# Kernel tuning notes

Measured on AMD Instinct MI355X. Metric: run time of the kernel, lower is better.

## Reference

```python
import jax, jax.numpy as jnp
import numpy as np

DIM = 256      # C
TOPK = 32      # topk_win_num
WIN = 8        # winSize
G = 64         # g (shift group size); 4*G == DIM here


def setup_inputs() -> dict:
    key = jax.random.key(0)
    k0, k1, k2, k3 = jax.random.split(key, 4)
    B, Nt, Ns, C = 32, 256, 4096, DIM
    z = jax.random.normal(k0, (B, Nt, C), jnp.float32)
    x = jax.random.normal(k1, (B, Ns, C), jnp.float32)
    # shift_op_down: Conv2d(C, 4g, 1) -> weight [4g, C]; shift_op_up: Conv2d(4g, C, 1)
    Wd = jax.random.normal(k2, (4 * G, C), jnp.float32) * 0.05
    bd = jnp.zeros((4 * G,), jnp.float32)
    Wu = jax.random.normal(k3, (C, 4 * G), jnp.float32) * 0.05
    bu = jnp.zeros((C,), jnp.float32)
    return {"z": z, "x": x, "Wd": Wd, "bd": bd, "Wu": Wu, "bu": bu}


def reference(z, x, Wd, bd, Wu, bu):
    B, Nt, C = z.shape
    Ns = x.shape[1]
    hs = int(np.sqrt(Ns))
    wn = hs // WIN          # windows per side
    wsa = WIN * WIN         # tokens per window
    K = TOPK

    # AdaptiveMaxPool2d((1,1)) over template tokens -> global max per channel
    z_max = jnp.max(z, axis=1)                               # [B, C]
    sim = jnp.einsum('bc,bnc->bn', z_max, x) / C             # [B, Ns]
    # per-window mean similarity
    sim = sim.reshape(B, wn, WIN, wn, WIN).transpose(0, 1, 3, 2, 4)
    sim = sim.reshape(B, wn * wn, wsa).mean(-1)              # [B, wn*wn]
    idx = jax.lax.top_k(sim, K)[1]                           # [B, K]

    # windowed view of search tokens: [B, wn*wn, wsa, C]
    x_win = x.reshape(B, wn, WIN, wn, WIN, C).transpose(0, 1, 3, 2, 4, 5)
    x_win = x_win.reshape(B, wn * wn, wsa, C)
    x_sel = jnp.take_along_axis(x_win, idx[:, :, None, None], axis=1)  # [B, K, wsa, C]

    xe = x_sel.reshape(B * K, WIN, WIN, C)                   # NHWC per selected window
    t = xe @ Wd.T + bd                                       # 1x1 conv down -> [n, h, w, 4G]

    # 4-direction spatial shift by 1 (zero fill), one channel group per direction
    g0, g1, g2, g3 = t[..., :G], t[..., G:2 * G], t[..., 2 * G:3 * G], t[..., 3 * G:]
    s0 = jnp.pad(g0[:, :, 1:, :], ((0, 0), (0, 0), (0, 1), (0, 0)))  # shift left  (W)
    s1 = jnp.pad(g1[:, :, :-1, :], ((0, 0), (0, 0), (1, 0), (0, 0)))  # shift right (W)
    s2 = jnp.pad(g2[:, 1:, :, :], ((0, 0), (0, 1), (0, 0), (0, 0)))  # shift up    (H)
    s3 = jnp.pad(g3[:, :-1, :, :], ((0, 0), (1, 0), (0, 0), (0, 0)))  # shift down  (H)
    sh = jnp.concatenate([s0, s1, s2, s3], axis=-1)          # [n, h, w, 4G]

    up = sh @ Wu.T + bu                                      # 1x1 conv up -> [n, h, w, C]
    out = (xe + up).reshape(B, K * WIN * WIN, C)             # [B, K*wsa, C]
    return out
```

## Files before the change

kernel.cpp:

```cpp
#include <hip/hip_runtime.h>
#include <hip/hip_bf16.h>

#define C_DIM 256
#define B_SZ 32
#define NS 4096
#define NT_Z 256
#define TOPK_K 32
#define NWIN 64
#define WTOK 64

typedef __attribute__((ext_vector_type(8))) short short8;
typedef __attribute__((ext_vector_type(4))) float f32x4;

static __device__ inline unsigned short f2b(float f) {
  union { float f; unsigned int u; } x; x.f = f;
  unsigned int u = x.u;
  return (unsigned short)((u + 0x7FFFu + ((u >> 16) & 1u)) >> 16);
}
static __device__ inline float b2f(unsigned int h16) {
  union { unsigned int u; float f; } x; x.u = h16 << 16;
  return x.f;
}

__global__ void prep_kernel(const float* __restrict__ Wd, const float* __restrict__ Wu,
                            unsigned short* __restrict__ Wdb, unsigned short* __restrict__ Wub,
                            const float* __restrict__ z, float* __restrict__ zpart) {
  int blk = blockIdx.x;
  if (blk < 64) {
    int i = blk * 256 + threadIdx.x;
    float4 a = ((const float4*)Wd)[i];
    float4 c = ((const float4*)Wu)[i];
    ushort4 ha, hc;
    ha.x = f2b(a.x); ha.y = f2b(a.y); ha.z = f2b(a.z); ha.w = f2b(a.w);
    hc.x = f2b(c.x); hc.y = f2b(c.y); hc.z = f2b(c.z); hc.w = f2b(c.w);
    ((ushort4*)Wdb)[i] = ha;
    ((ushort4*)Wub)[i] = hc;
  } else {
    int i = blk - 64;
    int b = i >> 3, ch = i & 7;
    int c = threadIdx.x;
    const float* p = z + ((size_t)b * NT_Z + ch * 32) * C_DIM + c;
    float m = p[0];
    for (int n = 1; n < 32; ++n) m = fmaxf(m, p[(size_t)n * C_DIM]);
    zpart[(size_t)i * C_DIM + c] = m;
  }
}

__global__ __launch_bounds__(256) void winscore_kernel(const float* __restrict__ x,
                                                       const float* __restrict__ zpart,
                                                       float* __restrict__ score) {
  int b = blockIdx.x >> 6;
  int w = blockIdx.x & 63;
  int wy = w >> 3, wx = w & 7;

  __shared__ float zs[C_DIM];
  {
    float m = zpart[(size_t)(b * 8) * C_DIM + threadIdx.x];
    #pragma unroll
    for (int ch = 1; ch < 8; ++ch)
      m = fmaxf(m, zpart[(size_t)(b * 8 + ch) * C_DIM + threadIdx.x]);
    zs[threadIdx.x] = m;
  }
  __syncthreads();

  int wv = threadIdx.x >> 6;
  int ln = threadIdx.x & 63;

  float a0 = 0.f, a1 = 0.f, a2 = 0.f, a3 = 0.f;
  for (int t = 0; t < 16; ++t) {
    int tok = wv * 16 + t;
    int iy = tok >> 3, ix = tok & 7;
    int n = (wy * 8 + iy) * 64 + wx * 8 + ix;
    const float4 v = *(const float4*)(x + ((size_t)b * NS + n) * C_DIM + ln * 4);
    a0 += v.x; a1 += v.y; a2 += v.z; a3 += v.w;
  }
  const float4 z4 = ((const float4*)zs)[ln];
  float p = a0 * z4.x + a1 * z4.y + a2 * z4.z + a3 * z4.w;
  for (int off = 32; off >= 1; off >>= 1) p += __shfl_xor(p, off);

  __shared__ float wsum[4];
  if (ln == 0) wsum[wv] = p;
  __syncthreads();
  if (threadIdx.x == 0) score[blockIdx.x] = wsum[0] + wsum[1] + wsum[2] + wsum[3];
}

__global__ __launch_bounds__(256, 2) void fused_win(
    const float* __restrict__ x, const float* __restrict__ score,
    const unsigned short* __restrict__ Wdb, const unsigned short* __restrict__ Wub,
    const float* __restrict__ bd, const float* __restrict__ bu,
    float* __restrict__ out)
{
  __shared__ unsigned short xe_s[WTOK * C_DIM];
  __shared__ unsigned short t_s[WTOK * C_DIM];
  __shared__ float sc[NWIN];
  __shared__ int wsel_s;

  const int bk = blockIdx.x;
  const int b = bk >> 5;
  const int kk = bk & 31;
  const int tid = threadIdx.x;

  if (tid < NWIN) sc[tid] = score[b * NWIN + tid];
  __syncthreads();
  if (tid < NWIN) {
    float v = sc[tid];
    int rank = 0;
    #pragma unroll
    for (int j = 0; j < NWIN; ++j) {
      float sj = sc[j];
      rank += (sj > v) || (sj == v && j < tid);
    }
    if (rank == kk) wsel_s = tid;
  }
  __syncthreads();
  const int wsel = wsel_s;
  const int wy = wsel >> 3, wx = wsel & 7;

  const int wv = tid >> 6;
  const int ln = tid & 63;
  const int lr = ln & 15;
  const int lg = ln >> 4;

  const unsigned short* wdbase = Wdb + ((wv * 4) * 16 + lr) * C_DIM + lg * 8;
  const unsigned short* wubase = Wub + ((wv * 4) * 16 + lr) * C_DIM + lg * 8;

  short8 wreg[8][4];
  #pragma unroll
  for (int ks = 0; ks < 8; ++ks)
    #pragma unroll
    for (int nt = 0; nt < 4; ++nt)
      wreg[ks][nt] = *(const short8*)(wdbase + nt * 16 * C_DIM + ks * 32);

  {
    const int c4 = tid & 63;
    const int m0 = tid >> 6;
    const float* xb = x + (size_t)b * NS * C_DIM + c4 * 4;
    float4 xv[16];
    #pragma unroll
    for (int i = 0; i < 16; ++i) {
      int m = m0 + i * 4;
      int n = (wy * 8 + (m >> 3)) * 64 + wx * 8 + (m & 7);
      xv[i] = *(const float4*)(xb + (size_t)n * C_DIM);
    }
    #pragma unroll
    for (int i = 0; i < 16; ++i) {
      int m = m0 + i * 4;
      ushort4 h;
      h.x = f2b(xv[i].x); h.y = f2b(xv[i].y); h.z = f2b(xv[i].z); h.w = f2b(xv[i].w);
      int byteoff = m * 512 + ((c4 * 8) ^ ((m & 7) << 4));
      *(ushort4*)((char*)xe_s + byteoff) = h;
    }
  }
  __syncthreads();

  f32x4 acc[4][4];
  #pragma unroll
  for (int a = 0; a < 4; ++a)
    #pragma unroll
    for (int n2 = 0; n2 < 4; ++n2) acc[a][n2] = (f32x4){0.f, 0.f, 0.f, 0.f};

  #pragma unroll
  for (int ks = 0; ks < 8; ++ks) {
    const int kb = ks * 64 + lg * 16;
    short8 af[4];
    #pragma unroll
    for (int mt = 0; mt < 4; ++mt) {
      int m = mt * 16 + lr;
      af[mt] = *(const short8*)((const char*)xe_s + m * 512 + (kb ^ ((m & 7) << 4)));
    }
    #pragma unroll
    for (int mt = 0; mt < 4; ++mt)
      #pragma unroll
      for (int nt = 0; nt < 4; ++nt)
        acc[mt][nt] = __builtin_amdgcn_mfma_f32_16x16x32_bf16(af[mt], wreg[ks][nt], acc[mt][nt], 0, 0, 0);
  }

  #pragma unroll
  for (int nt = 0; nt < 4; ++nt) {
    int o = wv * 64 + nt * 16 + lr;
    float bdv = bd[o];
    #pragma unroll
    for (int mt = 0; mt < 4; ++mt) {
      #pragma unroll
      for (int r = 0; r < 4; ++r) {
        int m = mt * 16 + lg * 4 + r;
        float v = acc[mt][nt][r] + bdv;
        *(unsigned short*)((char*)t_s + m * 512 + ((o * 2) ^ ((m & 7) << 4))) = f2b(v);
      }
    }
  }

  short8 wreg2[8][4];
  #pragma unroll
  for (int ks = 0; ks < 8; ++ks)
    #pragma unroll
    for (int nt = 0; nt < 4; ++nt)
      wreg2[ks][nt] = *(const short8*)(wubase + nt * 16 * C_DIM + ks * 32);

  __syncthreads();

  f32x4 acc2[4][4];
  #pragma unroll
  for (int a = 0; a < 4; ++a)
    #pragma unroll
    for (int n2 = 0; n2 < 4; ++n2) acc2[a][n2] = (f32x4){0.f, 0.f, 0.f, 0.f};

  #pragma unroll
  for (int ks = 0; ks < 8; ++ks) {
    const int g = ks >> 1;
    const int dd = ((g & 1) ? -1 : 1) * ((g & 2) ? 8 : 1);
    const int kb = ks * 64 + lg * 16;
    short8 af[4];
    #pragma unroll
    for (int mt = 0; mt < 4; ++mt) {
      int m = mt * 16 + lr;
      int pos = (g & 2) ? (m >> 3) : (m & 7);
      bool ok = (g & 1) ? (pos > 0) : (pos < 7);
      int ms = m + dd;
      ms = ms < 0 ? 0 : (ms > 63 ? 63 : ms);
      short8 v = *(const short8*)((const char*)t_s + ms * 512 + (kb ^ ((ms & 7) << 4)));
      const short8 zed = {0, 0, 0, 0, 0, 0, 0, 0};
      af[mt] = ok ? v : zed;
    }
    #pragma unroll
    for (int mt = 0; mt < 4; ++mt)
      #pragma unroll
      for (int nt = 0; nt < 4; ++nt)
        acc2[mt][nt] = __builtin_amdgcn_mfma_f32_16x16x32_bf16(af[mt], wreg2[ks][nt], acc2[mt][nt], 0, 0, 0);
  }

  const size_t obase = (size_t)bk * WTOK * C_DIM;
  #pragma unroll
  for (int nt = 0; nt < 4; ++nt) {
    int c = wv * 64 + nt * 16 + lr;
    float buv = bu[c];
    #pragma unroll
    for (int mt = 0; mt < 4; ++mt) {
      #pragma unroll
      for (int r = 0; r < 4; ++r) {
        int m = mt * 16 + lg * 4 + r;
        unsigned int xb =
            *(const unsigned short*)((const char*)xe_s + m * 512 + ((c * 2) ^ ((m & 7) << 4)));
        out[obase + (size_t)m * C_DIM + c] = b2f(xb) + acc2[mt][nt][r] + buv;
      }
    }
  }
}

extern "C" void kernel_launch(void* const* d_in, const int* in_sizes, int n_in,
                              void* d_out, int out_size, void* d_ws, size_t ws_size,
                              hipStream_t stream) {
  const float* z  = (const float*)d_in[0];
  const float* x  = (const float*)d_in[1];
  const float* Wd = (const float*)d_in[2];
  const float* bd = (const float*)d_in[3];
  const float* Wu = (const float*)d_in[4];
  const float* bu = (const float*)d_in[5];
  float* out = (float*)d_out;

  char* ws = (char*)d_ws;
  unsigned short* Wdb = (unsigned short*)(ws);
  unsigned short* Wub = (unsigned short*)(ws + 131072);
  float* zpart = (float*)(ws + 262144);
  float* score = (float*)(ws + 524288);

  hipLaunchKernelGGL(prep_kernel, dim3(320), dim3(256), 0, stream, Wd, Wu, Wdb, Wub, z, zpart);
  hipLaunchKernelGGL(winscore_kernel, dim3(B_SZ * NWIN), dim3(256), 0, stream, x, zpart, score);
  hipLaunchKernelGGL(fused_win, dim3(B_SZ * TOPK_K), dim3(256), 0, stream,
                     x, score, Wdb, Wub, bd, bu, out);
}
```

Before: 82.46 us.

## Fold down and up projections into per-direction combined weight matrices

Since the shift is linear and each channel group shifts in one direction, the up and down 1x1 convs are composed into four combined 256x256 matrices, one per shift direction, in the prep kernel. The fused kernel then runs a single K=1024 GEMM over shifted copies of the input tile. This drops the intermediate t_s buffer, its store/sync, and one GEMM stage, and halves shared memory. In exchange the main GEMM does twice the MFMA work (K=1024 vs two K=256 stages), streams 512KB of combined weights from global/L2 per block, and changes rounding because the bf16 intermediate is gone.

```diff
diff --git a/kernel.cpp b/kernel.cpp
--- a/kernel.cpp
+++ b/kernel.cpp
@@ -22,23 +22,36 @@
   return x.f;
 }
 
-__global__ void prep_kernel(const float* __restrict__ Wd, const float* __restrict__ Wu,
-                            unsigned short* __restrict__ Wdb, unsigned short* __restrict__ Wub,
-                            const float* __restrict__ z, float* __restrict__ zpart) {
+__global__ __launch_bounds__(256) void prep_kernel(
+    const float* __restrict__ Wd, const float* __restrict__ Wu,
+    const float* __restrict__ bd,
+    unsigned short* __restrict__ Eb, float* __restrict__ B2,
+    const float* __restrict__ z, float* __restrict__ zpart) {
   int blk = blockIdx.x;
-  if (blk < 64) {
-    int i = blk * 256 + threadIdx.x;
-    float4 a = ((const float4*)Wd)[i];
-    float4 c = ((const float4*)Wu)[i];
-    ushort4 ha, hc;
-    ha.x = f2b(a.x); ha.y = f2b(a.y); ha.z = f2b(a.z); ha.w = f2b(a.w);
-    hc.x = f2b(c.x); hc.y = f2b(c.y); hc.z = f2b(c.z); hc.w = f2b(c.w);
-    ((ushort4*)Wdb)[i] = ha;
-    ((ushort4*)Wub)[i] = hc;
+  int tid = threadIdx.x;
+  if (blk < 256) {
+    int co = blk, ci = tid;
+    __shared__ float wu_s[C_DIM];
+    wu_s[ci] = b2f(f2b(Wu[(size_t)co * C_DIM + ci]));
+    __syncthreads();
+    #pragma unroll
+    for (int g = 0; g < 4; ++g) {
+      float acc = 0.f;
+      #pragma unroll 8
+      for (int j = 0; j < 64; ++j)
+        acc += wu_s[g * 64 + j] * b2f(f2b(Wd[(size_t)(g * 64 + j) * C_DIM + ci]));
+      Eb[(size_t)(g * 256 + co) * C_DIM + ci] = f2b(acc);
+    }
+    if (ci < 4) {
+      int g = ci;
+      float s = 0.f;
+      for (int j = 0; j < 64; ++j) s += bd[g * 64 + j] * wu_s[g * 64 + j];
+      B2[g * 256 + co] = s;
+    }
   } else {
-    int i = blk - 64;
+    int i = blk - 256;
     int b = i >> 3, ch = i & 7;
-    int c = threadIdx.x;
+    int c = tid;
     const float* p = z + ((size_t)b * NT_Z + ch * 32) * C_DIM + c;
     float m = p[0];
     for (int n = 1; n < 32; ++n) m = fmaxf(m, p[(size_t)n * C_DIM]);
@@ -84,14 +97,12 @@
   if (threadIdx.x == 0) score[blockIdx.x] = wsum[0] + wsum[1] + wsum[2] + wsum[3];
 }
 
-__global__ __launch_bounds__(256, 2) void fused_win(
+__global__ __launch_bounds__(256) void fused_win(
     const float* __restrict__ x, const float* __restrict__ score,
-    const unsigned short* __restrict__ Wdb, const unsigned short* __restrict__ Wub,
-    const float* __restrict__ bd, const float* __restrict__ bu,
-    float* __restrict__ out)
+    const unsigned short* __restrict__ Eb, const float* __restrict__ B2,
+    const float* __restrict__ bu, float* __restrict__ out)
 {
   __shared__ unsigned short xe_s[WTOK * C_DIM];
-  __shared__ unsigned short t_s[WTOK * C_DIM];
   __shared__ float sc[NWIN];
   __shared__ int wsel_s;
 
@@ -115,21 +126,6 @@
   __syncthreads();
   const int wsel = wsel_s;
   const int wy = wsel >> 3, wx = wsel & 7;
-
-  const int wv = tid >> 6;
-  const int ln = tid & 63;
-  const int lr = ln & 15;
-  const int lg = ln >> 4;
-
-  const unsigned short* wdbase = Wdb + ((wv * 4) * 16 + lr) * C_DIM + lg * 8;
-  const unsigned short* wubase = Wub + ((wv * 4) * 16 + lr) * C_DIM + lg * 8;
-
-  short8 wreg[8][4];
-  #pragma unroll
-  for (int ks = 0; ks < 8; ++ks)
-    #pragma unroll
-    for (int nt = 0; nt < 4; ++nt)
-      wreg[ks][nt] = *(const short8*)(wdbase + nt * 16 * C_DIM + ks * 32);
 
   {
     const int c4 = tid & 63;
@@ -153,6 +149,13 @@
   }
   __syncthreads();
 
+  const int wv = tid >> 6;
+  const int ln = tid & 63;
+  const int lr = ln & 15;
+  const int lg = ln >> 4;
+
+  const unsigned short* ebase = Eb + (size_t)(wv * 64 + lr) * C_DIM + lg * 8;
+
   f32x4 acc[4][4];
   #pragma unroll
   for (int a = 0; a < 4; ++a)
@@ -160,73 +163,33 @@
     for (int n2 = 0; n2 < 4; ++n2) acc[a][n2] = (f32x4){0.f, 0.f, 0.f, 0.f};
 
   #pragma unroll
-  for (int ks = 0; ks < 8; ++ks) {
-    const int kb = ks * 64 + lg * 16;
-    short8 af[4];
-    #pragma unroll
-    for (int mt = 0; mt < 4; ++mt) {
-      int m = mt * 16 + lr;
-      af[mt] = *(const short8*)((const char*)xe_s + m * 512 + (kb ^ ((m & 7) << 4)));
-    }
-    #pragma unroll
-    for (int mt = 0; mt < 4; ++mt)
+  for (int g = 0; g < 4; ++g) {
+    const int dd = (g == 0) ? 1 : (g == 1) ? -1 : (g == 2) ? 8 : -8;
+    #pragma unroll
+    for (int ks = 0; ks < 8; ++ks) {
+      short8 bf[4];
       #pragma unroll
       for (int nt = 0; nt < 4; ++nt)
-        acc[mt][nt] = __builtin_amdgcn_mfma_f32_16x16x32_bf16(af[mt], wreg[ks][nt], acc[mt][nt], 0, 0, 0);
-  }
-
-  #pragma unroll
-  for (int nt = 0; nt < 4; ++nt) {
-    int o = wv * 64 + nt * 16 + lr;
-    float bdv = bd[o];
-    #pragma unroll
-    for (int mt = 0; mt < 4; ++mt) {
-      #pragma unroll
-      for (int r = 0; r < 4; ++r) {
-        int m = mt * 16 + lg * 4 + r;
-        float v = acc[mt][nt][r] + bdv;
-        *(unsigned short*)((char*)t_s + m * 512 + ((o * 2) ^ ((m & 7) << 4))) = f2b(v);
+        bf[nt] = *(const short8*)(ebase + (size_t)g * 65536 + nt * 16 * C_DIM + ks * 32);
+      const int kb = ks * 64 + lg * 16;
+      short8 af[4];
+      #pragma unroll
+      for (int mt = 0; mt < 4; ++mt) {
+        int m = mt * 16 + lr;
+        int pos = (g >= 2) ? (m >> 3) : (m & 7);
+        bool ok = (g & 1) ? (pos > 0) : (pos < 7);
+        int ms = m + dd;
+        ms = ms < 0 ? 0 : (ms > 63 ? 63 : ms);
+        short8 v = *(const short8*)((const char*)xe_s + ms * 512 + (kb ^ ((ms & 7) << 4)));
+        const short8 zed = {0, 0, 0, 0, 0, 0, 0, 0};
+        af[mt] = ok ? v : zed;
       }
-    }
-  }
-
-  short8 wreg2[8][4];
-  #pragma unroll
-  for (int ks = 0; ks < 8; ++ks)
-    #pragma unroll
-    for (int nt = 0; nt < 4; ++nt)
-      wreg2[ks][nt] = *(const short8*)(wubase + nt * 16 * C_DIM + ks * 32);
-
-  __syncthreads();
-
-  f32x4 acc2[4][4];
-  #pragma unroll
-  for (int a = 0; a < 4; ++a)
-    #pragma unroll
-    for (int n2 = 0; n2 < 4; ++n2) acc2[a][n2] = (f32x4){0.f, 0.f, 0.f, 0.f};
-
-  #pragma unroll
-  for (int ks = 0; ks < 8; ++ks) {
-    const int g = ks >> 1;
-    const int dd = ((g & 1) ? -1 : 1) * ((g & 2) ? 8 : 1);
-    const int kb = ks * 64 + lg * 16;
-    short8 af[4];
-    #pragma unroll
-    for (int mt = 0; mt < 4; ++mt) {
-      int m = mt * 16 + lr;
-      int pos = (g & 2) ? (m >> 3) : (m & 7);
-      bool ok = (g & 1) ? (pos > 0) : (pos < 7);
-      int ms = m + dd;
-      ms = ms < 0 ? 0 : (ms > 63 ? 63 : ms);
-      short8 v = *(const short8*)((const char*)t_s + ms * 512 + (kb ^ ((ms & 7) << 4)));
-      const short8 zed = {0, 0, 0, 0, 0, 0, 0, 0};
-      af[mt] = ok ? v : zed;
-    }
-    #pragma unroll
-    for (int mt = 0; mt < 4; ++mt)
-      #pragma unroll
-      for (int nt = 0; nt < 4; ++nt)
-        acc2[mt][nt] = __builtin_amdgcn_mfma_f32_16x16x32_bf16(af[mt], wreg2[ks][nt], acc2[mt][nt], 0, 0, 0);
+      #pragma unroll
+      for (int mt = 0; mt < 4; ++mt)
+        #pragma unroll
+        for (int nt = 0; nt < 4; ++nt)
+          acc[mt][nt] = __builtin_amdgcn_mfma_f32_16x16x32_bf16(af[mt], bf[nt], acc[mt][nt], 0, 0, 0);
+    }
   }
 
   const size_t obase = (size_t)bk * WTOK * C_DIM;
@@ -234,14 +197,19 @@
   for (int nt = 0; nt < 4; ++nt) {
     int c = wv * 64 + nt * 16 + lr;
     float buv = bu[c];
+    float b2v0 = B2[0 * 256 + c], b2v1 = B2[1 * 256 + c];
+    float b2v2 = B2[2 * 256 + c], b2v3 = B2[3 * 256 + c];
     #pragma unroll
     for (int mt = 0; mt < 4; ++mt) {
       #pragma unroll
       for (int r = 0; r < 4; ++r) {
         int m = mt * 16 + lg * 4 + r;
-        unsigned int xb =
+        int fx = m & 7, fy = m >> 3;
+        float bias = buv + (fx < 7 ? b2v0 : 0.f) + (fx > 0 ? b2v1 : 0.f)
+                         + (fy < 7 ? b2v2 : 0.f) + (fy > 0 ? b2v3 : 0.f);
+        unsigned int xr =
             *(const unsigned short*)((const char*)xe_s + m * 512 + ((c * 2) ^ ((m & 7) << 4)));
-        out[obase + (size_t)m * C_DIM + c] = b2f(xb) + acc2[mt][nt][r] + buv;
+        out[obase + (size_t)m * C_DIM + c] = b2f(xr) + acc[mt][nt][r] + bias;
       }
     }
   }
@@ -259,13 +227,14 @@
   float* out = (float*)d_out;
 
   char* ws = (char*)d_ws;
-  unsigned short* Wdb = (unsigned short*)(ws);
-  unsigned short* Wub = (unsigned short*)(ws + 131072);
-  float* zpart = (float*)(ws + 262144);
-  float* score = (float*)(ws + 524288);
-
-  hipLaunchKernelGGL(prep_kernel, dim3(320), dim3(256), 0, stream, Wd, Wu, Wdb, Wub, z, zpart);
+  unsigned short* Eb = (unsigned short*)(ws);
+  float* B2    = (float*)(ws + 524288);
+  float* zpart = (float*)(ws + 528384);
+  float* score = (float*)(ws + 794624);
+
+  hipLaunchKernelGGL(prep_kernel, dim3(512), dim3(256), 0, stream,
+                     Wd, Wu, bd, Eb, B2, z, zpart);
   hipLaunchKernelGGL(winscore_kernel, dim3(B_SZ * NWIN), dim3(256), 0, stream, x, zpart, score);
   hipLaunchKernelGGL(fused_win, dim3(B_SZ * TOPK_K), dim3(256), 0, stream,
-                     x, score, Wdb, Wub, bd, bu, out);
-}
+                     x, score, Eb, B2, bu, out);
+}
```

New measurement: 119.0 us. +44.3%, slower.
